# Optimization experiments

Measured on AMD Instinct MI355X. Metric: run time of the kernel, lower is better.

## Reference

```python
import jax, jax.numpy as jnp
import numpy as np

H_IMG = 224
W_IMG = 224
CHUNK = 128   # triangles rasterized per scan step
EPS = 1e-8
N_VERTS = 6890
N_FACES = 13776
BATCH = 2


def setup_inputs() -> dict:
    key = jax.random.key(0)
    k0, k1, k2 = jax.random.split(key, 3)
    # vertices in front of the camera (z ~ 2.5) so triangles project into the image
    v = jax.random.normal(k0, (BATCH, N_VERTS, 3), jnp.float32) * 0.3 + jnp.array([0.0, 0.0, 2.5], jnp.float32)
    vc = jax.random.uniform(k1, (N_VERTS, 3), dtype=jnp.float32)          # per-vertex colors
    f = jax.random.randint(k2, (N_FACES, 3), 0, N_VERTS, dtype=jnp.int32)  # triangle list
    bgcolor = jnp.zeros((3,), jnp.float32)
    camera_f = jnp.array([500.0, 500.0], jnp.float32)
    camera_c = jnp.array([112.0, 112.0], jnp.float32)
    camera_t = jnp.zeros((3,), jnp.float32)
    camera_rt = jnp.zeros((3,), jnp.float32)
    return {"v": v, "vc": vc, "bgcolor": bgcolor, "camera_f": camera_f,
            "camera_c": camera_c, "camera_t": camera_t, "camera_rt": camera_rt, "f": f}


def _rodrigues(r):
    # axis-angle -> rotation matrix, safe at r = 0
    th = jnp.sqrt(jnp.sum(r * r) + 1e-12)
    k = r / th
    kx, ky, kz = k[0], k[1], k[2]
    z = jnp.zeros_like(kx)
    K = jnp.stack([jnp.stack([z, -kz, ky]),
                   jnp.stack([kz, z, -kx]),
                   jnp.stack([-ky, kx, z])])
    c, s = jnp.cos(th), jnp.sin(th)
    return c * jnp.eye(3, dtype=r.dtype) + (1.0 - c) * jnp.outer(k, k) + s * K


def _edge(ax, ay, bx, by, px, py):
    # signed area of (a, b, p) * 2
    return (bx - ax) * (py - ay) - (by - ay) * (px - ax)


def _rasterize(uv, zc, vc, faces, bgcolor, height, width):
    """Z-buffered rasterization with perspective-correct barycentric color interp.
    uv: [V,2] screen coords, zc: [V] camera-space depth, vc: [V,C], faces: [F,3]."""
    F, C = faces.shape[0], vc.shape[-1]
    pad = (-F) % CHUNK
    faces_p = jnp.concatenate([faces, jnp.zeros((pad, 3), faces.dtype)], 0)
    fmask = jnp.concatenate([jnp.ones((F,), bool), jnp.zeros((pad,), bool)])
    faces_p = faces_p.reshape(-1, CHUNK, 3)
    fmask = fmask.reshape(-1, CHUNK)

    xs = jnp.arange(width, dtype=jnp.float32) + 0.5
    ys = jnp.arange(height, dtype=jnp.float32) + 0.5
    px, py = jnp.meshgrid(xs, ys)              # [H,W] pixel centers
    cx = px.ravel()[None, :]                    # [1,HW]
    cy = py.ravel()[None, :]
    HW = height * width
    ar = jnp.arange(HW)

    def step(carry, inp):
        zbuf, col = carry
        fc, fm = inp                            # [K,3] int, [K] bool
        p = uv[fc]                              # [K,3,2]
        zt = zc[fc]                             # [K,3]
        x0, y0 = p[:, 0, 0:1], p[:, 0, 1:2]
        x1, y1 = p[:, 1, 0:1], p[:, 1, 1:2]
        x2, y2 = p[:, 2, 0:1], p[:, 2, 1:2]
        w0 = _edge(x1, y1, x2, y2, cx, cy)      # [K,HW]
        w1 = _edge(x2, y2, x0, y0, cx, cy)
        w2 = _edge(x0, y0, x1, y1, cx, cy)
        area = _edge(x0, y0, x1, y1, x2, y2)    # [K,1]
        nz = jnp.abs(area) > EPS
        inv_area = jnp.where(nz, 1.0 / jnp.where(nz, area, 1.0), 0.0)
        b0, b1, b2 = w0 * inv_area, w1 * inv_area, w2 * inv_area
        inside = (b0 >= 0) & (b1 >= 0) & (b2 >= 0)
        zvalid = jnp.all(zt > EPS, axis=1, keepdims=True)
        valid = inside & zvalid & nz & fm[:, None]
        zt_s = jnp.maximum(zt, EPS)
        inv_z = b0 / zt_s[:, 0:1] + b1 / zt_s[:, 1:2] + b2 / zt_s[:, 2:3]
        zp = jnp.where(valid & (inv_z > EPS), 1.0 / jnp.maximum(inv_z, EPS), jnp.inf)
        idx = jnp.argmin(zp, axis=0)            # nearest triangle per pixel in chunk
        zmin = zp[idx, ar]                      # [HW]
        hit = jnp.isfinite(zmin)
        zmin_s = jnp.where(hit, zmin, 1.0)
        bb = jnp.stack([b0, b1, b2], -1)[idx, ar]   # [HW,3]
        fsel = fc[idx]                          # [HW,3]
        zsel = jnp.maximum(zt[idx], EPS)        # [HW,3]
        csel = vc[fsel]                         # [HW,3,C]
        pc = bb / zsel                          # perspective-correct weights / z
        newcol = jnp.einsum('pk,pkc->pc', pc, csel) * zmin_s[:, None]
        upd = hit & (zmin < zbuf)
        zbuf = jnp.where(upd, zmin_s, zbuf)
        col = jnp.where(upd[:, None], newcol, col)
        return (zbuf, col), None

    zbuf0 = jnp.full((HW,), jnp.inf, jnp.float32)
    col0 = jnp.broadcast_to(bgcolor.astype(jnp.float32), (HW, C))
    (zbuf, col), _ = jax.lax.scan(step, (zbuf0, col0), (faces_p, fmask))
    return col.reshape(height, width, C)


def reference(v, vc, bgcolor, camera_f, camera_c, camera_t, camera_rt, f):
    R = _rodrigues(camera_rt)
    vcam = jnp.einsum('bvj,ij->bvi', v, R) + camera_t   # [B,V,3]
    z = vcam[..., 2]
    zs = jnp.maximum(z, EPS)
    uv = vcam[..., :2] / zs[..., None] * camera_f + camera_c  # pinhole projection
    render = jax.vmap(lambda uv_b, z_b: _rasterize(uv_b, z_b, vc, f, bgcolor, H_IMG, W_IMG))
    return render(uv, z)                                   # [B,H,W,C]
```

## Files before the change

### kernel.cpp

```cpp
#include <hip/hip_runtime.h>
#include <math.h>

#define H_IMG 224
#define W_IMG 224
#define HW (H_IMG * W_IMG)
#define EPSF 1e-8f
#define NV 6890
#define NF 13776
#define NB 2
#define FCHUNK 128
#define NCHUNK ((NF + FCHUNK - 1) / FCHUNK)
#define FPAD (NCHUNK * FCHUNK)
#define NBUCK 1024
#define CHDR_STRIDE 128
#define KEY_INIT 0x7F800000FFFFFFFFULL

#define OFF_VERTS 0u
#define OFF_ZBU   220672u
#define OFF_ZBS   331008u
#define OFF_BBS   441600u
#define OFF_GMS   883968u
#define OFF_OIS   2653440u
#define OFF_INV   2764032u
#define OFF_CHDR  2874368u
#define OFF_CNT   2875392u
#define OFF_OFFS  2883584u
#define OFF_KEY   2891776u

__device__ inline unsigned long long shfl_xor_u64(unsigned long long v, int m) {
  unsigned lo = (unsigned)v, hi = (unsigned)(v >> 32);
  lo = __shfl_xor(lo, m);
  hi = __shfl_xor(hi, m);
  return ((unsigned long long)hi << 32) | lo;
}

__global__ void proj_kernel(const float* __restrict__ v,
                            const float* __restrict__ cf,
                            const float* __restrict__ cc,
                            const float* __restrict__ ct,
                            const float* __restrict__ crt,
                            float4* __restrict__ verts) {
  int i = blockIdx.x * blockDim.x + threadIdx.x;
  if (i >= NB * NV) return;
  float r0 = crt[0], r1 = crt[1], r2 = crt[2];
  float ss = __fadd_rn(__fadd_rn(__fmul_rn(r0, r0), __fmul_rn(r1, r1)), __fmul_rn(r2, r2));
  float th = sqrtf(__fadd_rn(ss, 1e-12f));
  float kx = r0 / th, ky = r1 / th, kz = r2 / th;
  float c = cosf(th), s = sinf(th), oc = 1.0f - c;
  float R00 = c + oc * kx * kx,      R01 = oc * kx * ky - s * kz, R02 = oc * kx * kz + s * ky;
  float R10 = oc * ky * kx + s * kz, R11 = c + oc * ky * ky,      R12 = oc * ky * kz - s * kx;
  float R20 = oc * kz * kx - s * ky, R21 = oc * kz * ky + s * kx, R22 = c + oc * kz * kz;
  float x = v[i * 3 + 0], y = v[i * 3 + 1], z = v[i * 3 + 2];
  float xc = R00 * x + R01 * y + R02 * z + ct[0];
  float yc = R10 * x + R11 * y + R12 * z + ct[1];
  float zc = R20 * x + R21 * y + R22 * z + ct[2];
  float zs = fmaxf(zc, EPSF);
  float u = __fadd_rn(__fmul_rn(xc / zs, cf[0]), cc[0]);
  float w = __fadd_rn(__fmul_rn(yc / zs, cf[1]), cc[1]);
  verts[i] = make_float4(u, w, zc, 0.0f);
}

__global__ void init_kernel(unsigned long long* __restrict__ keybuf,
                            float* __restrict__ zbS, float4* __restrict__ bbS,
                            unsigned* __restrict__ chdr, unsigned* __restrict__ cnt) {
  int t = blockIdx.x * blockDim.x + threadIdx.x;
  if (t < NB * HW) keybuf[t] = KEY_INIT;
  if (t < NB * FPAD) {
    zbS[t] = 3e30f;
    bbS[t] = make_float4(1e30f, -1e30f, 1e30f, -1e30f);
  }
  if (t < NB * CHDR_STRIDE) chdr[t] = 0x7F800000u;
  if (t < NB * NBUCK) cnt[t] = 0u;
}

__global__ void zb_kernel(const int* __restrict__ f, const float4* __restrict__ verts,
                          float* __restrict__ zbU, unsigned* __restrict__ cnt) {
  int i = blockIdx.x * blockDim.x + threadIdx.x;
  if (i >= NB * NF) return;
  int b = i / NF, fi = i - b * NF;
  int i0 = f[fi * 3 + 0], i1 = f[fi * 3 + 1], i2 = f[fi * 3 + 2];
  float4 p0 = verts[b * NV + i0], p1 = verts[b * NV + i1], p2 = verts[b * NV + i2];
  float area = __fsub_rn(__fmul_rn(__fsub_rn(p1.x, p0.x), __fsub_rn(p2.y, p0.y)),
                         __fmul_rn(__fsub_rn(p1.y, p0.y), __fsub_rn(p2.x, p0.x)));
  bool nz = fabsf(area) > EPSF;
  bool zv = (p0.z > EPSF) && (p1.z > EPSF) && (p2.z > EPSF);
  bool ok = nz && zv;
  float zb;
  if (!ok) {
    zb = 3e30f;
  } else {
    float minz = fminf(fminf(fmaxf(p0.z, EPSF), fmaxf(p1.z, EPSF)), fmaxf(p2.z, EPSF));
    float M = fmaxf(fmaxf(fmaxf(fabsf(p0.x), fabsf(p0.y)), fmaxf(fabsf(p1.x), fabsf(p1.y))),
                    fmaxf(fabsf(p2.x), fabsf(p2.y)));
    float werr = (2.0f * M) * (M + 256.0f) * 6e-7f;
    bool tight = (3.0f * werr) <= (5e-4f * fabsf(area));
    zb = tight ? __fmul_rn(minz, 0.999f) : 0.0f;
  }
  zbU[i] = zb;
  int bucket = (int)fminf(fmaxf(zb * 256.0f, 0.0f), (float)(NBUCK - 1));
  atomicAdd(&cnt[b * NBUCK + bucket], 1u);
}

__global__ __launch_bounds__(1024) void scan_kernel(const unsigned* __restrict__ cnt,
                                                    unsigned* __restrict__ offs) {
  __shared__ unsigned s[NBUCK];
  int t = threadIdx.x;
  int b = blockIdx.x;
  unsigned v = cnt[b * NBUCK + t];
  s[t] = v;
  __syncthreads();
  unsigned acc = v;
  for (int d = 1; d < NBUCK; d <<= 1) {
    unsigned add = (t >= d) ? s[t - d] : 0u;
    __syncthreads();
    acc += add;
    s[t] = acc;
    __syncthreads();
  }
  offs[b * NBUCK + t] = acc - v;
}

__global__ void scatter_kernel(const int* __restrict__ f, const float4* __restrict__ verts,
                               const float* __restrict__ zbU, unsigned* __restrict__ offs,
                               float* __restrict__ zbS, float4* __restrict__ bbS,
                               float4* __restrict__ gmS, int* __restrict__ oiS,
                               int* __restrict__ inv, unsigned* __restrict__ chdr) {
  int i = blockIdx.x * blockDim.x + threadIdx.x;
  if (i >= NB * NF) return;
  int b = i / NF, fi = i - b * NF;
  float zb = zbU[i];
  int bucket = (int)fminf(fmaxf(zb * 256.0f, 0.0f), (float)(NBUCK - 1));
  unsigned pos = atomicAdd(&offs[b * NBUCK + bucket], 1u);
  int i0 = f[fi * 3 + 0], i1 = f[fi * 3 + 1], i2 = f[fi * 3 + 2];
  float4 p0 = verts[b * NV + i0], p1 = verts[b * NV + i1], p2 = verts[b * NV + i2];
  float x0 = p0.x, y0 = p0.y, z0 = p0.z;
  float x1 = p1.x, y1 = p1.y, z1 = p1.z;
  float x2 = p2.x, y2 = p2.y, z2 = p2.z;
  float area = __fsub_rn(__fmul_rn(__fsub_rn(x1, x0), __fsub_rn(y2, y0)),
                         __fmul_rn(__fsub_rn(y1, y0), __fsub_rn(x2, x0)));
  bool nz = fabsf(area) > EPSF;
  float inv_area = nz ? (1.0f / area) : 0.0f;
  bool zv = (z0 > EPSF) && (z1 > EPSF) && (z2 > EPSF);
  bool ok = nz && zv;
  float zz0 = ok ? fmaxf(z0, EPSF) : 1e30f;
  float zz1 = ok ? fmaxf(z1, EPSF) : 1e30f;
  float zz2 = ok ? fmaxf(z2, EPSF) : 1e30f;
  size_t sp_ = (size_t)b * FPAD + pos;
  zbS[sp_] = zb;
  bbS[sp_] = make_float4(fminf(fminf(x0, x1), x2), fmaxf(fmaxf(x0, x1), x2),
                         fminf(fminf(y0, y1), y2), fmaxf(fmaxf(y0, y1), y2));
  gmS[sp_ * 4 + 0] = make_float4(__fsub_rn(x2, x1), __fsub_rn(y2, y1), x1, y1);
  gmS[sp_ * 4 + 1] = make_float4(__fsub_rn(x0, x2), __fsub_rn(y0, y2), x2, y2);
  gmS[sp_ * 4 + 2] = make_float4(__fsub_rn(x1, x0), __fsub_rn(y1, y0), x0, y0);
  gmS[sp_ * 4 + 3] = make_float4(zz0, zz1, zz2, inv_area);
  oiS[sp_] = fi;
  inv[i] = (int)pos;
  atomicMin(&chdr[b * CHDR_STRIDE + (int)(pos / FCHUNK)], __float_as_uint(zb));
}

__global__ __launch_bounds__(CHDR_STRIDE) void suffix_kernel(unsigned* __restrict__ chdr) {
  __shared__ unsigned s[CHDR_STRIDE];
  int t = threadIdx.x, b = blockIdx.x;
  s[t] = chdr[b * CHDR_STRIDE + t];
  __syncthreads();
  for (int d = 1; d < CHDR_STRIDE; d <<= 1) {
    unsigned v = (t + d < CHDR_STRIDE) ? s[t + d] : 0x7F800000u;
    __syncthreads();
    s[t] = (v < s[t]) ? v : s[t];
    __syncthreads();
  }
  chdr[b * CHDR_STRIDE + t] = s[t];
}

__global__ __launch_bounds__(256) void raster_kernel(
    const unsigned* __restrict__ chdr,
    const float* __restrict__ zbS,
    const float4* __restrict__ bbS,
    const float4* __restrict__ gmS,
    const int* __restrict__ oiS,
    unsigned long long* __restrict__ keybuf) {
  int b = blockIdx.z;
  int w = threadIdx.x >> 6;
  int lane = threadIdx.x & 63;
  int slot = lane & 3;
  int p = lane >> 2;
  int wx = (blockIdx.x * 2 + (w & 1)) * 4;
  int wy = (blockIdx.y * 2 + (w >> 1)) * 4;
  int x = wx + (p & 3);
  int y = wy + (p >> 2);
  float px = (float)x + 0.5f, py = (float)y + 0.5f;
  float tx0 = (float)wx + 0.5f, tx1 = (float)wx + 3.5f;
  float ty0 = (float)wy + 0.5f, ty1 = (float)wy + 3.5f;
  const unsigned* chdrB = chdr + b * CHDR_STRIDE;
  const float*  zbB = zbS + (size_t)b * FPAD;
  const float4* bbB = bbS + (size_t)b * FPAD;
  const float4* gmB = gmS + (size_t)b * FPAD * 4;
  const int*    oiB = oiS + (size_t)b * FPAD;

  unsigned long long bestKey = KEY_INIT;

  for (int c = 0; c < NCHUNK; ++c) {
    float bz = __uint_as_float((unsigned)(bestKey >> 32));
    float comb = fminf(bz, __shfl_xor(bz, 1));
    comb = fminf(comb, __shfl_xor(comb, 2));
    float czb = __uint_as_float(chdrB[c]);
    if (!__any(czb <= comb)) break;
    float combMax = fmaxf(comb, __shfl_xor(comb, 4));
    combMax = fmaxf(combMax, __shfl_xor(combMax, 8));
    combMax = fmaxf(combMax, __shfl_xor(combMax, 16));
    combMax = fmaxf(combMax, __shfl_xor(combMax, 32));
    int base = c * FCHUNK;
    #pragma unroll
    for (int h = 0; h < FCHUNK / 64; ++h) {
      int fbase = base + h * 64;
      float zb_lane = zbB[fbase + lane];
      float4 bb = bbB[fbase + lane];
      bool pass = (zb_lane <= combMax) &&
                  (bb.x <= tx1) && (bb.y >= tx0) &&
                  (bb.z <= ty1) && (bb.w >= ty0);
      unsigned long long m = __ballot(pass);
      unsigned long long mm = m;
      while (mm) {
        int bit = __builtin_ctzll(mm);
        int g = bit & ~3;
        mm &= ~(0xFULL << g);
        if ((m >> (g + slot)) & 1) {
          int fi = fbase + g + slot;
          const float4* gm = &gmB[(size_t)fi * 4];
          float4 q0 = gm[0], q1 = gm[1], q2 = gm[2], q3 = gm[3];
          float w0 = __fsub_rn(__fmul_rn(q0.x, __fsub_rn(py, q0.w)),
                               __fmul_rn(q0.y, __fsub_rn(px, q0.z)));
          float w1 = __fsub_rn(__fmul_rn(q1.x, __fsub_rn(py, q1.w)),
                               __fmul_rn(q1.y, __fsub_rn(px, q1.z)));
          float w2 = __fsub_rn(__fmul_rn(q2.x, __fsub_rn(py, q2.w)),
                               __fmul_rn(q2.y, __fsub_rn(px, q2.z)));
          float b0 = __fmul_rn(w0, q3.w);
          float b1 = __fmul_rn(w1, q3.w);
          float b2 = __fmul_rn(w2, q3.w);
          if (b0 >= 0.0f && b1 >= 0.0f && b2 >= 0.0f) {
            float invz = __fadd_rn(__fadd_rn(b0 / q3.x, b1 / q3.y), b2 / q3.z);
            if (invz > EPSF) {
              float zp = 1.0f / invz;
              unsigned long long key =
                  ((unsigned long long)__float_as_uint(zp) << 32) | (unsigned)oiB[fi];
              if (key < bestKey) bestKey = key;
            }
          }
        }
      }
    }
  }

  unsigned long long o = shfl_xor_u64(bestKey, 1);
  if (o < bestKey) bestKey = o;
  o = shfl_xor_u64(bestKey, 2);
  if (o < bestKey) bestKey = o;
  if (slot == 0 && bestKey != KEY_INIT)
    atomicMin(&keybuf[(size_t)b * HW + (size_t)y * W_IMG + x], bestKey);
}

__global__ void shade_kernel(const unsigned long long* __restrict__ keybuf,
                             const float4* __restrict__ gmS,
                             const int* __restrict__ inv,
                             const int* __restrict__ f,
                             const float* __restrict__ vc,
                             const float* __restrict__ bg,
                             float* __restrict__ out) {
  int p = blockIdx.x * blockDim.x + threadIdx.x;
  if (p >= NB * HW) return;
  int b = p / HW, pix = p - b * HW;
  int y = pix / W_IMG, x = pix - y * W_IMG;
  float px = (float)x + 0.5f, py = (float)y + 0.5f;
  unsigned long long key = keybuf[p];
  float o0, o1, o2;
  if (key != KEY_INIT) {
    int best = (int)(unsigned)(key & 0xFFFFFFFFu);
    float zmin = __uint_as_float((unsigned)(key >> 32));
    int pos = inv[b * NF + best];
    const float4* g = &gmS[((size_t)b * FPAD + pos) * 4];
    float4 q0 = g[0], q1 = g[1], q2 = g[2], q3 = g[3];
    float w0 = __fsub_rn(__fmul_rn(q0.x, __fsub_rn(py, q0.w)),
                         __fmul_rn(q0.y, __fsub_rn(px, q0.z)));
    float w1 = __fsub_rn(__fmul_rn(q1.x, __fsub_rn(py, q1.w)),
                         __fmul_rn(q1.y, __fsub_rn(px, q1.z)));
    float w2 = __fsub_rn(__fmul_rn(q2.x, __fsub_rn(py, q2.w)),
                         __fmul_rn(q2.y, __fsub_rn(px, q2.z)));
    float b0 = __fmul_rn(w0, q3.w), b1 = __fmul_rn(w1, q3.w), b2 = __fmul_rn(w2, q3.w);
    float pc0 = b0 / q3.x, pc1 = b1 / q3.y, pc2 = b2 / q3.z;
    int i0 = f[best * 3 + 0], i1 = f[best * 3 + 1], i2 = f[best * 3 + 2];
    const float* c0p = vc + (size_t)i0 * 3;
    const float* c1p = vc + (size_t)i1 * 3;
    const float* c2p = vc + (size_t)i2 * 3;
    o0 = __fmul_rn(__fadd_rn(__fadd_rn(__fmul_rn(pc0, c0p[0]), __fmul_rn(pc1, c1p[0])),
                             __fmul_rn(pc2, c2p[0])), zmin);
    o1 = __fmul_rn(__fadd_rn(__fadd_rn(__fmul_rn(pc0, c0p[1]), __fmul_rn(pc1, c1p[1])),
                             __fmul_rn(pc2, c2p[1])), zmin);
    o2 = __fmul_rn(__fadd_rn(__fadd_rn(__fmul_rn(pc0, c0p[2]), __fmul_rn(pc1, c1p[2])),
                             __fmul_rn(pc2, c2p[2])), zmin);
  } else {
    o0 = bg[0]; o1 = bg[1]; o2 = bg[2];
  }
  size_t o = (size_t)p * 3;
  out[o + 0] = o0;
  out[o + 1] = o1;
  out[o + 2] = o2;
}

extern "C" void kernel_launch(void* const* d_in, const int* in_sizes, int n_in,
                              void* d_out, int out_size, void* d_ws, size_t ws_size,
                              hipStream_t stream) {
  const float* v   = (const float*)d_in[0];
  const float* vc  = (const float*)d_in[1];
  const float* bg  = (const float*)d_in[2];
  const float* cf  = (const float*)d_in[3];
  const float* cc  = (const float*)d_in[4];
  const float* ct  = (const float*)d_in[5];
  const float* crt = (const float*)d_in[6];
  const int*   f   = (const int*)d_in[7];
  float* out = (float*)d_out;
  char* ws = (char*)d_ws;

  float4*   verts = (float4*)(ws + OFF_VERTS);
  float*    zbU   = (float*)(ws + OFF_ZBU);
  float*    zbS   = (float*)(ws + OFF_ZBS);
  float4*   bbS   = (float4*)(ws + OFF_BBS);
  float4*   gmS   = (float4*)(ws + OFF_GMS);
  int*      oiS   = (int*)(ws + OFF_OIS);
  int*      inv   = (int*)(ws + OFF_INV);
  unsigned* chdr  = (unsigned*)(ws + OFF_CHDR);
  unsigned* cnt   = (unsigned*)(ws + OFF_CNT);
  unsigned* offs  = (unsigned*)(ws + OFF_OFFS);
  unsigned long long* keybuf = (unsigned long long*)(ws + OFF_KEY);

  hipLaunchKernelGGL(init_kernel, dim3((NB * HW + 255) / 256), dim3(256), 0, stream,
                     keybuf, zbS, bbS, chdr, cnt);
  hipLaunchKernelGGL(proj_kernel, dim3((NB * NV + 255) / 256), dim3(256), 0, stream,
                     v, cf, cc, ct, crt, verts);
  hipLaunchKernelGGL(zb_kernel, dim3((NB * NF + 255) / 256), dim3(256), 0, stream,
                     f, verts, zbU, cnt);
  hipLaunchKernelGGL(scan_kernel, dim3(NB), dim3(1024), 0, stream, cnt, offs);
  hipLaunchKernelGGL(scatter_kernel, dim3((NB * NF + 255) / 256), dim3(256), 0, stream,
                     f, verts, zbU, offs, zbS, bbS, gmS, oiS, inv, chdr);
  hipLaunchKernelGGL(suffix_kernel, dim3(NB), dim3(CHDR_STRIDE), 0, stream, chdr);
  hipLaunchKernelGGL(raster_kernel, dim3(W_IMG / 8, H_IMG / 8, NB),
                     dim3(256), 0, stream, chdr, zbS, bbS, gmS, oiS, keybuf);
  hipLaunchKernelGGL(shade_kernel, dim3((NB * HW + 255) / 256), dim3(256), 0, stream,
                     keybuf, gmS, inv, f, vc, bg, out);
}
```

Baseline: 333.9 us.

## Split raster chunk loop across four blocks, fuse init/proj, warp-shuffle scan

```diff
diff --git a/kernel.cpp b/kernel.cpp
--- a/kernel.cpp
+++ b/kernel.cpp
@@ -11,6 +11,7 @@
 #define FCHUNK 128
 #define NCHUNK ((NF + FCHUNK - 1) / FCHUNK)
 #define FPAD (NCHUNK * FCHUNK)
+#define NSPLIT 4
 #define NBUCK 1024
 #define CHDR_STRIDE 128
 #define KEY_INIT 0x7F800000FFFFFFFFULL
@@ -34,43 +35,41 @@
   return ((unsigned long long)hi << 32) | lo;
 }
 
-__global__ void proj_kernel(const float* __restrict__ v,
-                            const float* __restrict__ cf,
-                            const float* __restrict__ cc,
-                            const float* __restrict__ ct,
-                            const float* __restrict__ crt,
-                            float4* __restrict__ verts) {
+__global__ void proj_init_kernel(const float* __restrict__ v,
+                                 const float* __restrict__ cf,
+                                 const float* __restrict__ cc,
+                                 const float* __restrict__ ct,
+                                 const float* __restrict__ crt,
+                                 float4* __restrict__ verts,
+                                 unsigned long long* __restrict__ keybuf,
+                                 float* __restrict__ zbS, float4* __restrict__ bbS,
+                                 unsigned* __restrict__ chdr, unsigned* __restrict__ cnt) {
   int i = blockIdx.x * blockDim.x + threadIdx.x;
-  if (i >= NB * NV) return;
-  float r0 = crt[0], r1 = crt[1], r2 = crt[2];
-  float ss = __fadd_rn(__fadd_rn(__fmul_rn(r0, r0), __fmul_rn(r1, r1)), __fmul_rn(r2, r2));
-  float th = sqrtf(__fadd_rn(ss, 1e-12f));
-  float kx = r0 / th, ky = r1 / th, kz = r2 / th;
-  float c = cosf(th), s = sinf(th), oc = 1.0f - c;
-  float R00 = c + oc * kx * kx,      R01 = oc * kx * ky - s * kz, R02 = oc * kx * kz + s * ky;
-  float R10 = oc * ky * kx + s * kz, R11 = c + oc * ky * ky,      R12 = oc * ky * kz - s * kx;
-  float R20 = oc * kz * kx - s * ky, R21 = oc * kz * ky + s * kx, R22 = c + oc * kz * kz;
-  float x = v[i * 3 + 0], y = v[i * 3 + 1], z = v[i * 3 + 2];
-  float xc = R00 * x + R01 * y + R02 * z + ct[0];
-  float yc = R10 * x + R11 * y + R12 * z + ct[1];
-  float zc = R20 * x + R21 * y + R22 * z + ct[2];
-  float zs = fmaxf(zc, EPSF);
-  float u = __fadd_rn(__fmul_rn(xc / zs, cf[0]), cc[0]);
-  float w = __fadd_rn(__fmul_rn(yc / zs, cf[1]), cc[1]);
-  verts[i] = make_float4(u, w, zc, 0.0f);
-}
-
-__global__ void init_kernel(unsigned long long* __restrict__ keybuf,
-                            float* __restrict__ zbS, float4* __restrict__ bbS,
-                            unsigned* __restrict__ chdr, unsigned* __restrict__ cnt) {
-  int t = blockIdx.x * blockDim.x + threadIdx.x;
-  if (t < NB * HW) keybuf[t] = KEY_INIT;
-  if (t < NB * FPAD) {
-    zbS[t] = 3e30f;
-    bbS[t] = make_float4(1e30f, -1e30f, 1e30f, -1e30f);
-  }
-  if (t < NB * CHDR_STRIDE) chdr[t] = 0x7F800000u;
-  if (t < NB * NBUCK) cnt[t] = 0u;
+  if (i < NB * NV) {
+    float r0 = crt[0], r1 = crt[1], r2 = crt[2];
+    float ss = __fadd_rn(__fadd_rn(__fmul_rn(r0, r0), __fmul_rn(r1, r1)), __fmul_rn(r2, r2));
+    float th = sqrtf(__fadd_rn(ss, 1e-12f));
+    float kx = r0 / th, ky = r1 / th, kz = r2 / th;
+    float c = cosf(th), s = sinf(th), oc = 1.0f - c;
+    float R00 = c + oc * kx * kx,      R01 = oc * kx * ky - s * kz, R02 = oc * kx * kz + s * ky;
+    float R10 = oc * ky * kx + s * kz, R11 = c + oc * ky * ky,      R12 = oc * ky * kz - s * kx;
+    float R20 = oc * kz * kx - s * ky, R21 = oc * kz * ky + s * kx, R22 = c + oc * kz * kz;
+    float x = v[i * 3 + 0], y = v[i * 3 + 1], z = v[i * 3 + 2];
+    float xc = R00 * x + R01 * y + R02 * z + ct[0];
+    float yc = R10 * x + R11 * y + R12 * z + ct[1];
+    float zc = R20 * x + R21 * y + R22 * z + ct[2];
+    float zs = fmaxf(zc, EPSF);
+    float u = __fadd_rn(__fmul_rn(xc / zs, cf[0]), cc[0]);
+    float w = __fadd_rn(__fmul_rn(yc / zs, cf[1]), cc[1]);
+    verts[i] = make_float4(u, w, zc, 0.0f);
+  }
+  if (i < NB * HW) keybuf[i] = KEY_INIT;
+  if (i < NB * FPAD) {
+    zbS[i] = 3e30f;
+    bbS[i] = make_float4(1e30f, -1e30f, 1e30f, -1e30f);
+  }
+  if (i < NB * CHDR_STRIDE) chdr[i] = 0x7F800000u;
+  if (i < NB * NBUCK) cnt[i] = 0u;
 }
 
 __global__ void zb_kernel(const int* __restrict__ f, const float4* __restrict__ verts,
@@ -103,21 +102,30 @@
 
 __global__ __launch_bounds__(1024) void scan_kernel(const unsigned* __restrict__ cnt,
                                                     unsigned* __restrict__ offs) {
-  __shared__ unsigned s[NBUCK];
-  int t = threadIdx.x;
-  int b = blockIdx.x;
+  __shared__ unsigned wsum[16];
+  int t = threadIdx.x, b = blockIdx.x;
+  int lane = t & 63, wid = t >> 6;
   unsigned v = cnt[b * NBUCK + t];
-  s[t] = v;
+  unsigned acc = v;
+  #pragma unroll
+  for (int d = 1; d < 64; d <<= 1) {
+    unsigned n = __shfl_up(acc, d);
+    if (lane >= d) acc += n;
+  }
+  if (lane == 63) wsum[wid] = acc;
   __syncthreads();
-  unsigned acc = v;
-  for (int d = 1; d < NBUCK; d <<= 1) {
-    unsigned add = (t >= d) ? s[t - d] : 0u;
-    __syncthreads();
-    acc += add;
-    s[t] = acc;
-    __syncthreads();
-  }
-  offs[b * NBUCK + t] = acc - v;
+  if (t < 16) {
+    unsigned wv = wsum[t];
+    #pragma unroll
+    for (int d = 1; d < 16; d <<= 1) {
+      unsigned n = __shfl_up(wv, d, 16);
+      if (t >= d) wv += n;
+    }
+    wsum[t] = wv;
+  }
+  __syncthreads();
+  unsigned base = (wid > 0) ? wsum[wid - 1] : 0u;
+  offs[b * NBUCK + t] = base + acc - v;
 }
 
 __global__ void scatter_kernel(const int* __restrict__ f, const float4* __restrict__ verts,
@@ -179,7 +187,8 @@
     const float4* __restrict__ gmS,
     const int* __restrict__ oiS,
     unsigned long long* __restrict__ keybuf) {
-  int b = blockIdx.z;
+  int bz = blockIdx.z;
+  int b = bz >> 2, sp = bz & (NSPLIT - 1);
   int w = threadIdx.x >> 6;
   int lane = threadIdx.x & 63;
   int slot = lane & 3;
@@ -199,9 +208,9 @@
 
   unsigned long long bestKey = KEY_INIT;
 
-  for (int c = 0; c < NCHUNK; ++c) {
-    float bz = __uint_as_float((unsigned)(bestKey >> 32));
-    float comb = fminf(bz, __shfl_xor(bz, 1));
+  for (int c = sp; c < NCHUNK; c += NSPLIT) {
+    float bz_ = __uint_as_float((unsigned)(bestKey >> 32));
+    float comb = fminf(bz_, __shfl_xor(bz_, 1));
     comb = fminf(comb, __shfl_xor(comb, 2));
     float czb = __uint_as_float(chdrB[c]);
     if (!__any(czb <= comb)) break;
@@ -332,17 +341,15 @@
   unsigned* offs  = (unsigned*)(ws + OFF_OFFS);
   unsigned long long* keybuf = (unsigned long long*)(ws + OFF_KEY);
 
-  hipLaunchKernelGGL(init_kernel, dim3((NB * HW + 255) / 256), dim3(256), 0, stream,
-                     keybuf, zbS, bbS, chdr, cnt);
-  hipLaunchKernelGGL(proj_kernel, dim3((NB * NV + 255) / 256), dim3(256), 0, stream,
-                     v, cf, cc, ct, crt, verts);
+  hipLaunchKernelGGL(proj_init_kernel, dim3((NB * HW + 255) / 256), dim3(256), 0, stream,
+                     v, cf, cc, ct, crt, verts, keybuf, zbS, bbS, chdr, cnt);
   hipLaunchKernelGGL(zb_kernel, dim3((NB * NF + 255) / 256), dim3(256), 0, stream,
                      f, verts, zbU, cnt);
   hipLaunchKernelGGL(scan_kernel, dim3(NB), dim3(1024), 0, stream, cnt, offs);
   hipLaunchKernelGGL(scatter_kernel, dim3((NB * NF + 255) / 256), dim3(256), 0, stream,
                      f, verts, zbU, offs, zbS, bbS, gmS, oiS, inv, chdr);
   hipLaunchKernelGGL(suffix_kernel, dim3(NB), dim3(CHDR_STRIDE), 0, stream, chdr);
-  hipLaunchKernelGGL(raster_kernel, dim3(W_IMG / 8, H_IMG / 8, NB),
+  hipLaunchKernelGGL(raster_kernel, dim3(W_IMG / 8, H_IMG / 8, NB * NSPLIT),
                      dim3(256), 0, stream, chdr, zbS, bbS, gmS, oiS, keybuf);
   hipLaunchKernelGGL(shade_kernel, dim3((NB * HW + 255) / 256), dim3(256), 0, stream,
                      keybuf, gmS, inv, f, vc, bg, out);
```

New measurement: 381.2 us. 14.2% more time.
